# Kernel tuning notes

Measured on AMD Instinct MI355X. Metric: run time of the kernel, lower is better.

## Reference

```python
import jax, jax.numpy as jnp
import numpy as np

D_MODEL = 768
NUM_HEADS = 12
D_K = D_MODEL // NUM_HEADS


def setup_inputs() -> dict:
    key = jax.random.key(0)
    ks = jax.random.split(key, 12)
    B, S = 4, 2048
    s = 1.0 / np.sqrt(D_MODEL)
    inp = {
        "query": jax.random.normal(ks[0], (B, S, D_MODEL), jnp.float32),
        "key": jax.random.normal(ks[1], (B, S, D_MODEL), jnp.float32),
        "value": jax.random.normal(ks[2], (B, S, D_MODEL), jnp.float32),
        "Wq": jax.random.normal(ks[3], (D_MODEL, D_MODEL), jnp.float32) * s,
        "bq": jnp.zeros((D_MODEL,), jnp.float32),
        "Wk": jax.random.normal(ks[4], (D_MODEL, D_MODEL), jnp.float32) * s,
        "bk": jnp.zeros((D_MODEL,), jnp.float32),
        "Wv": jax.random.normal(ks[5], (D_MODEL, D_MODEL), jnp.float32) * s,
        "bv": jnp.zeros((D_MODEL,), jnp.float32),
        "Wo": jax.random.normal(ks[6], (D_MODEL, D_MODEL), jnp.float32) * s,
        "bo": jnp.zeros((D_MODEL,), jnp.float32),
    }
    return inp


def _split_heads(x):
    B, S, _ = x.shape
    return x.reshape(B, S, NUM_HEADS, D_K).transpose(0, 2, 1, 3)  # [B,H,S,Dk]


def reference(query, key, value, Wq, bq, Wk, bk, Wv, bv, Wo, bo):
    # Linear projections (torch nn.Linear: x @ W.T + b)
    Q = _split_heads(query @ Wq.T + bq)
    K = _split_heads(key @ Wk.T + bk)
    V = _split_heads(value @ Wv.T + bv)
    scale = 1.0 / jnp.sqrt(jnp.asarray(D_K, Q.dtype))
    scores = jnp.einsum("bhqd,bhkd->bhqk", Q, K) * scale  # [B,H,S,S]
    attn = jax.nn.softmax(scores, axis=-1)
    # dropout is identity in eval mode
    out = jnp.einsum("bhqk,bhkd->bhqd", attn, V)  # [B,H,S,Dk]
    B, H, S, Dk = out.shape
    out = out.transpose(0, 2, 1, 3).reshape(B, S, H * Dk)
    return out @ Wo.T + bo
```

## Files before the change

### kernel.cpp

```cpp
#include <hip/hip_runtime.h>
#include <hip/hip_bf16.h>

typedef _Float16 half8 __attribute__((ext_vector_type(8)));
typedef _Float16 h4 __attribute__((ext_vector_type(4)));
typedef __fp16 fp16x2 __attribute__((ext_vector_type(2)));
typedef float f32x4 __attribute__((ext_vector_type(4)));

#define D_MODEL 768
#define NUM_HEADS 12
#define D_K 64
#define SEQ 2048
#define BATCH 4
#define M_TOTAL (BATCH * SEQ)
#define W_ELEMS (D_MODEL * D_MODEL)
#define X_ELEMS (M_TOTAL * D_MODEL)
#define QSCALE 0.18033688011112042f
#define SOFF 4.0f

__device__ __forceinline__ void gll16(const _Float16* g, _Float16* l) {
    __builtin_amdgcn_global_load_lds(
        (const __attribute__((address_space(1))) unsigned int*)g,
        (__attribute__((address_space(3))) unsigned int*)l,
        16, 0, 0);
}

__device__ __forceinline__ void pk2(float a, float b, _Float16* out) {
    fp16x2 r = __builtin_amdgcn_cvt_pkrtz(a, b);
    out[0] = (_Float16)r[0];
    out[1] = (_Float16)r[1];
}

__global__ void convert_all(
    const float* __restrict__ w0, const float* __restrict__ w1,
    const float* __restrict__ w2, const float* __restrict__ w3,
    const float* __restrict__ x0, const float* __restrict__ x1,
    const float* __restrict__ x2, _Float16* __restrict__ dst)
{
    const size_t W4 = W_ELEMS / 4, X4 = X_ELEMS / 4;
    size_t i = (size_t)blockIdx.x * blockDim.x + threadIdx.x;
    const float* src;
    size_t off;
    if (i < 4 * W4) {
        size_t slab = i / W4;
        off = i - slab * W4;
        src = (slab == 0) ? w0 : (slab == 1) ? w1 : (slab == 2) ? w2 : w3;
    } else {
        size_t j = i - 4 * W4;
        size_t slab = j / X4;
        off = j - slab * X4;
        src = (slab == 0) ? x0 : (slab == 1) ? x1 : x2;
    }
    float4 f = ((const float4*)src)[off];
    h4 h;
    h[0] = (_Float16)f.x; h[1] = (_Float16)f.y;
    h[2] = (_Float16)f.z; h[3] = (_Float16)f.w;
    ((h4*)dst)[i] = h;
}

__global__ __launch_bounds__(256) void gemm_qkv(
    const _Float16* __restrict__ Xall, const _Float16* __restrict__ Wall,
    const float* __restrict__ bq, const float* __restrict__ bk, const float* __restrict__ bv,
    _Float16* __restrict__ Qo, _Float16* __restrict__ Ko, _Float16* __restrict__ Vto)
{
    __shared__ __align__(16) char smem[36864];
    _Float16* As = (_Float16*)smem;
    _Float16* Bs = As + 128 * 64;

    const int z = blockIdx.z;
    const _Float16* X = Xall + (size_t)z * X_ELEMS;
    const _Float16* W = Wall + (size_t)z * W_ELEMS;

    const int t = threadIdx.x;
    const int w = t >> 6;
    const int l = t & 63;
    const int ln = t & 15;
    const int quad = (t >> 4) & 3;
    const int wm = w >> 1, wn = w & 1;
    const int m0 = blockIdx.x * 128, n0 = blockIdx.y * 128;

    const int srow = l >> 3;
    const int scol = (l & 7) ^ srow;

    f32x4 acc[4][4] = {};

    for (int k0 = 0; k0 < D_MODEL; k0 += 64) {
#pragma unroll
        for (int jj = 0; jj < 4; ++jj) {
            int j = w * 4 + jj;
            int row = j * 8 + srow;
            gll16(X + (size_t)(m0 + row) * D_MODEL + k0 + scol * 8, As + j * 512);
            gll16(W + (size_t)(n0 + row) * D_MODEL + k0 + scol * 8, Bs + j * 512);
        }
        __syncthreads();

#pragma unroll
        for (int kk = 0; kk < 2; ++kk) {
            half8 a[4], b[4];
#pragma unroll
            for (int i = 0; i < 4; ++i) {
                int ra = wm * 64 + i * 16 + ln;
                int rb = wn * 64 + i * 16 + ln;
                a[i] = *(const half8*)&As[ra * 64 + (((kk * 4 + quad) ^ (ln & 7)) * 8)];
                b[i] = *(const half8*)&Bs[rb * 64 + (((kk * 4 + quad) ^ (ln & 7)) * 8)];
            }
            if (z <= 1) {
#pragma unroll
                for (int i = 0; i < 4; ++i)
#pragma unroll
                    for (int j2 = 0; j2 < 4; ++j2)
                        acc[i][j2] = __builtin_amdgcn_mfma_f32_16x16x32_f16(b[j2], a[i], acc[i][j2], 0, 0, 0);
            } else {
#pragma unroll
                for (int i = 0; i < 4; ++i)
#pragma unroll
                    for (int j2 = 0; j2 < 4; ++j2)
                        acc[i][j2] = __builtin_amdgcn_mfma_f32_16x16x32_f16(a[i], b[j2], acc[i][j2], 0, 0, 0);
            }
        }
        __syncthreads();
    }

    if (z <= 1) {
        const float* bias = (z == 0) ? bq : bk;
        _Float16* dst = (z == 0) ? Qo : Ko;
        const int head = (n0 + wn * 64) >> 6;
#pragma unroll
        for (int i = 0; i < 4; ++i) {
            int m = m0 + wm * 64 + i * 16 + ln;
            int b_ = m >> 11, s_ = m & 2047;
            _Float16* rowp = dst + ((size_t)((b_ * NUM_HEADS + head) * SEQ + s_)) * D_K;
#pragma unroll
            for (int j = 0; j < 4; ++j) {
                int dbase = j * 16 + quad * 4;
                f32x4 bn = *(const f32x4*)&bias[n0 + wn * 64 + dbase];
                h4 o;
#pragma unroll
                for (int r = 0; r < 4; ++r) {
                    float v = acc[i][j][r] + bn[r];
                    if (z == 0) v *= QSCALE;
                    o[r] = (_Float16)v;
                }
                *(h4*)&rowp[dbase] = o;
            }
        }
    } else {
        const float* bias = bv;
        _Float16* T = (_Float16*)smem + (size_t)w * (64 * 72);
#pragma unroll
        for (int i = 0; i < 4; ++i) {
#pragma unroll
            for (int j = 0; j < 4; ++j) {
                float bn = bias[n0 + wn * 64 + j * 16 + ln];
                h4 hh;
#pragma unroll
                for (int r = 0; r < 4; ++r) hh[r] = (_Float16)(acc[i][j][r] + bn);
                *(h4*)&T[(j * 16 + ln) * 72 + i * 16 + quad * 4] = hh;
            }
        }
        const int b_ = m0 >> 11;
        const int s0 = (m0 & 2047) + wm * 64;
        const int head = (n0 >> 6) + wn;
        _Float16* base = Vto + (size_t)(b_ * NUM_HEADS + head) * D_K * SEQ + s0;
#pragma unroll
        for (int r8 = 0; r8 < 8; ++r8) {
            int nl = r8 * 8 + (l >> 3);
            half8 v = *(const half8*)&T[nl * 72 + (l & 7) * 8];
            *(half8*)(base + (size_t)nl * SEQ + (l & 7) * 8) = v;
        }
    }
}

__global__ __launch_bounds__(256) void attn(
    const _Float16* __restrict__ Qg, const _Float16* __restrict__ Kg,
    const _Float16* __restrict__ Vtg, _Float16* __restrict__ ctx)
{
    __shared__ __align__(16) _Float16 Ks[64 * 64];
    __shared__ __align__(16) _Float16 Vs[64 * 64];

    const int t = threadIdx.x;
    const int w = t >> 6;
    const int l = t & 63;
    const int ln = t & 15;
    const int quad = (t >> 4) & 3;
    const int bh = blockIdx.y;
    const int q0 = blockIdx.x * 128 + w * 32;

    const _Float16* Qh = Qg + (size_t)bh * SEQ * D_K;
    const _Float16* Kh = Kg + (size_t)bh * SEQ * D_K;
    const _Float16* Vh = Vtg + (size_t)bh * D_K * SEQ;

    const int srow = l >> 3;
    const int scol = (l & 7) ^ srow;
    const int j0 = w * 2, j1 = w * 2 + 1;
    const _Float16* Ksrc0 = Kh + (size_t)(j0 * 8 + srow) * D_K + scol * 8;
    const _Float16* Ksrc1 = Kh + (size_t)(j1 * 8 + srow) * D_K + scol * 8;
    const _Float16* Vsrc0 = Vh + (size_t)(j0 * 8 + srow) * SEQ + scol * 8;
    const _Float16* Vsrc1 = Vh + (size_t)(j1 * 8 + srow) * SEQ + scol * 8;

    half8 qf[2][2];
#pragma unroll
    for (int qt = 0; qt < 2; ++qt)
#pragma unroll
        for (int dh = 0; dh < 2; ++dh)
            qf[qt][dh] = *(const half8*)(Qh + (size_t)(q0 + qt * 16 + ln) * D_K + dh * 32 + quad * 8);

    f32x4 acc[2][4] = {};
    f32x4 lsum[2] = {};

    for (int c = 0; c < SEQ / 64; ++c) {
        const size_t koff = (size_t)c * 64 * D_K;
        const size_t voff = (size_t)c * 64;
        gll16(Ksrc0 + koff, &Ks[j0 * 512]);
        gll16(Ksrc1 + koff, &Ks[j1 * 512]);
        gll16(Vsrc0 + voff, &Vs[j0 * 512]);
        gll16(Vsrc1 + voff, &Vs[j1 * 512]);
        __syncthreads();

        h4 vfr[4][4];
#pragma unroll
        for (int dt = 0; dt < 4; ++dt)
#pragma unroll
            for (int kt = 0; kt < 4; ++kt) {
                int g = kt * 2 + (quad >> 1);
                vfr[dt][kt] = *(const h4*)&Vs[(dt * 16 + ln) * 64 + ((g ^ (ln & 7)) * 8) + (quad & 1) * 4];
            }

        h4 pB[2][4];
#pragma unroll
        for (int kt = 0; kt < 4; ++kt) {
            half8 kf0 = *(const half8*)&Ks[(kt * 16 + ln) * 64 + ((quad ^ (ln & 7)) * 8)];
            half8 kf1 = *(const half8*)&Ks[(kt * 16 + ln) * 64 + (((4 + quad) ^ (ln & 7)) * 8)];
#pragma unroll
            for (int qt = 0; qt < 2; ++qt) {
                f32x4 s = {-SOFF, -SOFF, -SOFF, -SOFF};
                s = __builtin_amdgcn_mfma_f32_16x16x32_f16(kf0, qf[qt][0], s, 0, 0, 0);
                s = __builtin_amdgcn_mfma_f32_16x16x32_f16(kf1, qf[qt][1], s, 0, 0, 0);
                f32x4 p;
                p[0] = __builtin_amdgcn_exp2f(s[0]);
                p[1] = __builtin_amdgcn_exp2f(s[1]);
                p[2] = __builtin_amdgcn_exp2f(s[2]);
                p[3] = __builtin_amdgcn_exp2f(s[3]);
                lsum[qt] += p;
                h4 h;
                pk2(p[0], p[1], (_Float16*)&h);
                pk2(p[2], p[3], ((_Float16*)&h) + 2);
                pB[qt][kt] = h;
            }
        }

#pragma unroll
        for (int dt = 0; dt < 4; ++dt)
#pragma unroll
            for (int kt = 0; kt < 4; ++kt) {
                acc[0][dt] = __builtin_amdgcn_mfma_f32_16x16x16f16(vfr[dt][kt], pB[0][kt], acc[0][dt], 0, 0, 0);
                acc[1][dt] = __builtin_amdgcn_mfma_f32_16x16x16f16(vfr[dt][kt], pB[1][kt], acc[1][dt], 0, 0, 0);
            }
        __syncthreads();
    }

    const int h = bh % NUM_HEADS, b = bh / NUM_HEADS;
#pragma unroll
    for (int qt = 0; qt < 2; ++qt) {
        float lp = lsum[qt][0] + lsum[qt][1] + lsum[qt][2] + lsum[qt][3];
        lp += __shfl_xor(lp, 16);
        lp += __shfl_xor(lp, 32);
        float rinv = __builtin_amdgcn_rcpf(lp);
        int q = q0 + qt * 16 + ln;
#pragma unroll
        for (int dt = 0; dt < 4; ++dt) {
            h4 o;
            o[0] = (_Float16)(acc[qt][dt][0] * rinv);
            o[1] = (_Float16)(acc[qt][dt][1] * rinv);
            o[2] = (_Float16)(acc[qt][dt][2] * rinv);
            o[3] = (_Float16)(acc[qt][dt][3] * rinv);
            *(h4*)&ctx[((size_t)(b * SEQ + q)) * D_MODEL + h * D_K + dt * 16 + quad * 4] = o;
        }
    }
}

__global__ __launch_bounds__(256) void gemm_out(
    const _Float16* __restrict__ A, const _Float16* __restrict__ W,
    const float* __restrict__ bo, float* __restrict__ out)
{
    __shared__ __align__(16) _Float16 As[128 * 64];
    __shared__ __align__(16) _Float16 Bs[128 * 64];

    const int t = threadIdx.x;
    const int w = t >> 6;
    const int l = t & 63;
    const int ln = t & 15;
    const int quad = (t >> 4) & 3;
    const int wm = w >> 1, wn = w & 1;
    const int m0 = blockIdx.x * 128, n0 = blockIdx.y * 128;

    const int srow = l >> 3;
    const int scol = (l & 7) ^ srow;

    f32x4 acc[4][4] = {};

    for (int k0 = 0; k0 < D_MODEL; k0 += 64) {
#pragma unroll
        for (int jj = 0; jj < 4; ++jj) {
            int j = w * 4 + jj;
            int row = j * 8 + srow;
            gll16(A + (size_t)(m0 + row) * D_MODEL + k0 + scol * 8, As + j * 512);
            gll16(W + (size_t)(n0 + row) * D_MODEL + k0 + scol * 8, Bs + j * 512);
        }
        __syncthreads();

#pragma unroll
        for (int kk = 0; kk < 2; ++kk) {
            half8 a[4], b[4];
#pragma unroll
            for (int i = 0; i < 4; ++i) {
                int ra = wm * 64 + i * 16 + ln;
                int rb = wn * 64 + i * 16 + ln;
                a[i] = *(const half8*)&As[ra * 64 + (((kk * 4 + quad) ^ (ln & 7)) * 8)];
                b[i] = *(const half8*)&Bs[rb * 64 + (((kk * 4 + quad) ^ (ln & 7)) * 8)];
            }
#pragma unroll
            for (int i = 0; i < 4; ++i)
#pragma unroll
                for (int j2 = 0; j2 < 4; ++j2)
                    acc[i][j2] = __builtin_amdgcn_mfma_f32_16x16x32_f16(b[j2], a[i], acc[i][j2], 0, 0, 0);
        }
        __syncthreads();
    }

#pragma unroll
    for (int i = 0; i < 4; ++i) {
        int m = m0 + wm * 64 + i * 16 + ln;
        float* rowp = out + (size_t)m * D_MODEL;
#pragma unroll
        for (int j = 0; j < 4; ++j) {
            int nb = n0 + wn * 64 + j * 16 + quad * 4;
            f32x4 o = acc[i][j] + *(const f32x4*)&bo[nb];
            *(f32x4*)&rowp[nb] = o;
        }
    }
}

extern "C" void kernel_launch(void* const* d_in, const int* in_sizes, int n_in,
                              void* d_out, int out_size, void* d_ws, size_t ws_size,
                              hipStream_t stream) {
    const float* query = (const float*)d_in[0];
    const float* key   = (const float*)d_in[1];
    const float* value = (const float*)d_in[2];
    const float* Wq = (const float*)d_in[3];
    const float* bq = (const float*)d_in[4];
    const float* Wk = (const float*)d_in[5];
    const float* bk = (const float*)d_in[6];
    const float* Wv = (const float*)d_in[7];
    const float* bv = (const float*)d_in[8];
    const float* Wo = (const float*)d_in[9];
    const float* bo = (const float*)d_in[10];
    float* out = (float*)d_out;

    _Float16* ws = (_Float16*)d_ws;
    _Float16* Wb  = ws;
    _Float16* Xb  = Wb + 4 * (size_t)W_ELEMS;
    _Float16* Qb  = Xb + 3 * (size_t)X_ELEMS;
    _Float16* Kb  = Qb + (size_t)X_ELEMS;
    _Float16* Vtb = Kb + (size_t)X_ELEMS;
    _Float16* ctx = Vtb + (size_t)X_ELEMS;

    const size_t total4 = (4 * (size_t)W_ELEMS + 3 * (size_t)X_ELEMS) / 4;
    convert_all<<<(int)(total4 / 256), 256, 0, stream>>>(
        Wq, Wk, Wv, Wo, query, key, value, Wb);

    gemm_qkv<<<dim3(M_TOTAL / 128, D_MODEL / 128, 3), 256, 0, stream>>>(
        Xb, Wb, bq, bk, bv, Qb, Kb, Vtb);

    attn<<<dim3(SEQ / 128, BATCH * NUM_HEADS), 256, 0, stream>>>(Qb, Kb, Vtb, ctx);

    gemm_out<<<dim3(M_TOTAL / 128, D_MODEL / 128), 256, 0, stream>>>(
        ctx, Wb + 3 * (size_t)W_ELEMS, bo, out);
}
```

Measured before the change: 271.2 us.

## Load K/V fragments directly from global memory in attention, drop LDS staging

The attention kernel no longer stages K and V tiles through shared memory with async global-to-LDS loads and block barriers. Each wave now loads its MFMA K and V operand fragments straight from global memory into registers. The grid is also transposed so that blocks for different heads sit next to each other in launch order, which may improve L2 reuse of K/V across blocks of the same head. This removes the LDS traffic and both __syncthreads per chunk, but each of the four waves now fetches the full K/V tile itself, raising global/L2 traffic and exposing load latency that LDS staging used to share.

```diff
diff --git a/kernel.cpp b/kernel.cpp
--- a/kernel.cpp
+++ b/kernel.cpp
@@ -174,29 +174,17 @@
     const _Float16* __restrict__ Qg, const _Float16* __restrict__ Kg,
     const _Float16* __restrict__ Vtg, _Float16* __restrict__ ctx)
 {
-    __shared__ __align__(16) _Float16 Ks[64 * 64];
-    __shared__ __align__(16) _Float16 Vs[64 * 64];
-
     const int t = threadIdx.x;
     const int w = t >> 6;
-    const int l = t & 63;
     const int ln = t & 15;
     const int quad = (t >> 4) & 3;
-    const int bh = blockIdx.y;
-    const int q0 = blockIdx.x * 128 + w * 32;
+    const int bh = blockIdx.x;
+    const int q0 = blockIdx.y * 128 + w * 32;
 
     const _Float16* Qh = Qg + (size_t)bh * SEQ * D_K;
     const _Float16* Kh = Kg + (size_t)bh * SEQ * D_K;
     const _Float16* Vh = Vtg + (size_t)bh * D_K * SEQ;
 
-    const int srow = l >> 3;
-    const int scol = (l & 7) ^ srow;
-    const int j0 = w * 2, j1 = w * 2 + 1;
-    const _Float16* Ksrc0 = Kh + (size_t)(j0 * 8 + srow) * D_K + scol * 8;
-    const _Float16* Ksrc1 = Kh + (size_t)(j1 * 8 + srow) * D_K + scol * 8;
-    const _Float16* Vsrc0 = Vh + (size_t)(j0 * 8 + srow) * SEQ + scol * 8;
-    const _Float16* Vsrc1 = Vh + (size_t)(j1 * 8 + srow) * SEQ + scol * 8;
-
     half8 qf[2][2];
 #pragma unroll
     for (int qt = 0; qt < 2; ++qt)
@@ -207,34 +195,31 @@
     f32x4 acc[2][4] = {};
     f32x4 lsum[2] = {};
 
+    const _Float16* kp = Kh + (size_t)ln * D_K + quad * 8;
+    const _Float16* vp = Vh + (size_t)ln * SEQ + quad * 4;
+
     for (int c = 0; c < SEQ / 64; ++c) {
-        const size_t koff = (size_t)c * 64 * D_K;
-        const size_t voff = (size_t)c * 64;
-        gll16(Ksrc0 + koff, &Ks[j0 * 512]);
-        gll16(Ksrc1 + koff, &Ks[j1 * 512]);
-        gll16(Vsrc0 + voff, &Vs[j0 * 512]);
-        gll16(Vsrc1 + voff, &Vs[j1 * 512]);
-        __syncthreads();
-
+        half8 kf[4][2];
+#pragma unroll
+        for (int kt = 0; kt < 4; ++kt) {
+            kf[kt][0] = *(const half8*)(kp + (size_t)(kt * 16) * D_K);
+            kf[kt][1] = *(const half8*)(kp + (size_t)(kt * 16) * D_K + 32);
+        }
         h4 vfr[4][4];
 #pragma unroll
         for (int dt = 0; dt < 4; ++dt)
 #pragma unroll
-            for (int kt = 0; kt < 4; ++kt) {
-                int g = kt * 2 + (quad >> 1);
-                vfr[dt][kt] = *(const h4*)&Vs[(dt * 16 + ln) * 64 + ((g ^ (ln & 7)) * 8) + (quad & 1) * 4];
-            }
+            for (int kt = 0; kt < 4; ++kt)
+                vfr[dt][kt] = *(const h4*)(vp + (size_t)(dt * 16) * SEQ + kt * 16);
 
         h4 pB[2][4];
 #pragma unroll
         for (int kt = 0; kt < 4; ++kt) {
-            half8 kf0 = *(const half8*)&Ks[(kt * 16 + ln) * 64 + ((quad ^ (ln & 7)) * 8)];
-            half8 kf1 = *(const half8*)&Ks[(kt * 16 + ln) * 64 + (((4 + quad) ^ (ln & 7)) * 8)];
 #pragma unroll
             for (int qt = 0; qt < 2; ++qt) {
                 f32x4 s = {-SOFF, -SOFF, -SOFF, -SOFF};
-                s = __builtin_amdgcn_mfma_f32_16x16x32_f16(kf0, qf[qt][0], s, 0, 0, 0);
-                s = __builtin_amdgcn_mfma_f32_16x16x32_f16(kf1, qf[qt][1], s, 0, 0, 0);
+                s = __builtin_amdgcn_mfma_f32_16x16x32_f16(kf[kt][0], qf[qt][0], s, 0, 0, 0);
+                s = __builtin_amdgcn_mfma_f32_16x16x32_f16(kf[kt][1], qf[qt][1], s, 0, 0, 0);
                 f32x4 p;
                 p[0] = __builtin_amdgcn_exp2f(s[0]);
                 p[1] = __builtin_amdgcn_exp2f(s[1]);
@@ -255,7 +240,9 @@
                 acc[0][dt] = __builtin_amdgcn_mfma_f32_16x16x16f16(vfr[dt][kt], pB[0][kt], acc[0][dt], 0, 0, 0);
                 acc[1][dt] = __builtin_amdgcn_mfma_f32_16x16x16f16(vfr[dt][kt], pB[1][kt], acc[1][dt], 0, 0, 0);
             }
-        __syncthreads();
+
+        kp += 64 * D_K;
+        vp += 64;
     }
 
     const int h = bh % NUM_HEADS, b = bh / NUM_HEADS;
@@ -371,7 +358,7 @@
     gemm_qkv<<<dim3(M_TOTAL / 128, D_MODEL / 128, 3), 256, 0, stream>>>(
         Xb, Wb, bq, bk, bv, Qb, Kb, Vtb);
 
-    attn<<<dim3(SEQ / 128, BATCH * NUM_HEADS), 256, 0, stream>>>(Qb, Kb, Vtb, ctx);
+    attn<<<dim3(BATCH * NUM_HEADS, SEQ / 128), 256, 0, stream>>>(Qb, Kb, Vtb, ctx);
 
     gemm_out<<<dim3(M_TOTAL / 128, D_MODEL / 128), 256, 0, stream>>>(
         ctx, Wb + 3 * (size_t)W_ELEMS, bo, out);
```

After: 470.5 us. 1.73x slower.
